# Optimization experiments

Hardware: AMD Instinct MI355X
Metric: run time of the kernel (lower is better)

The kernel has to match this reference:

```python
import jax, jax.numpy as jnp
import numpy as np

STRIDE = 1
PADDING = 1

def setup_inputs() -> dict:
    key = jax.random.key(0)
    k1, k2 = jax.random.split(key)
    X = jax.random.normal(k1, (32, 1024, 1024), dtype=jnp.float32)
    weight = jnp.array([[-1.0, -1.0, -1.0], [-1.0, 8.0, -1.0], [-1.0, -1.0, -1.0]], dtype=jnp.float32)
    return {"X": X, "weight": weight}

def reference(X, weight):
    # single-channel 2D cross-correlation, stride=1, padding=1
    # X: [B, M, N] -> lhs [B, 1, M, N]; weight: [u, v] -> rhs [1, 1, u, v]
    lhs = X[:, None, :, :]
    rhs = weight[None, None, :, :]
    out = jax.lax.conv_general_dilated(
        lhs, rhs,
        window_strides=(STRIDE, STRIDE),
        padding=[(PADDING, PADDING), (PADDING, PADDING)],
        dimension_numbers=("NCHW", "OIHW", "NCHW"),
    )
    return out[:, 0, :, :]  # [B, out_h, out_w]
```

## Files before the change

### kernel.cpp

```cpp
#include <hip/hip_runtime.h>

#define IMG_W 1024
#define IMG_H 1024
#define BATCH 32
#define ROWS 8

typedef float vfloat4 __attribute__((ext_vector_type(4)));

__global__ __launch_bounds__(256) void conv3x3_kernel(
    const float* __restrict__ X,
    const float* __restrict__ wt,
    float* __restrict__ out)
{
    const int y0 = blockIdx.x * ROWS;
    const int b  = blockIdx.y;
    const int c0 = threadIdx.x * 4;

    const float* img = X + (size_t)b * IMG_H * IMG_W;

    const float w0 = wt[0], w1 = wt[1], w2 = wt[2];
    const float w3 = wt[3], w4 = wt[4], w5 = wt[5];
    const float w6 = wt[6], w7 = wt[7], w8 = wt[8];

    float R[ROWS + 2][6];

#pragma unroll
    for (int i = 0; i < ROWS + 2; ++i) {
        const int ry = y0 + i - 1;
        if (ry >= 0 && ry < IMG_H) {
            const float* p = img + (size_t)ry * IMG_W + c0;
            const vfloat4 v = *(const vfloat4*)p;
            R[i][1] = v.x; R[i][2] = v.y; R[i][3] = v.z; R[i][4] = v.w;
            R[i][0] = (c0 > 0)         ? p[-1] : 0.f;
            R[i][5] = (c0 + 4 < IMG_W) ? p[4]  : 0.f;
        } else {
            R[i][0] = R[i][1] = R[i][2] = R[i][3] = R[i][4] = R[i][5] = 0.f;
        }
    }

    float* obase = out + ((size_t)b * IMG_H + y0) * IMG_W + c0;

#pragma unroll
    for (int i = 0; i < ROWS; ++i) {
        vfloat4 r;
#pragma unroll
        for (int j = 0; j < 4; ++j) {
            r[j] = w0 * R[i][j]     + w1 * R[i][j + 1]     + w2 * R[i][j + 2]
                 + w3 * R[i + 1][j] + w4 * R[i + 1][j + 1] + w5 * R[i + 1][j + 2]
                 + w6 * R[i + 2][j] + w7 * R[i + 2][j + 1] + w8 * R[i + 2][j + 2];
        }
        __builtin_nontemporal_store(r, (vfloat4*)(obase + (size_t)i * IMG_W));
    }
}

extern "C" void kernel_launch(void* const* d_in, const int* in_sizes, int n_in,
                              void* d_out, int out_size, void* d_ws, size_t ws_size,
                              hipStream_t stream) {
    const float* X  = (const float*)d_in[0];
    const float* wt = (const float*)d_in[1];
    float* out = (float*)d_out;

    dim3 grid(IMG_H / ROWS, BATCH);
    dim3 block(256);
    conv3x3_kernel<<<grid, block, 0, stream>>>(X, wt, out);
}
```

Before: 229.4 us.

## Use rolling 3-row register window with wave shuffles for column halos

Doubles rows per block to reduce vertical halo re-reads, replaces per-thread scalar halo loads with cross-lane shuffles (loading from memory only at wave edges), and keeps a rotating 3-row register buffer instead of all rows. It also raises the occupancy hint in launch bounds. This aims to cut redundant loads and register pressure, at the cost of fewer blocks in the grid and extra shuffle instructions.

```diff
diff --git a/kernel.cpp b/kernel.cpp
--- a/kernel.cpp
+++ b/kernel.cpp
@@ -3,18 +3,37 @@
 #define IMG_W 1024
 #define IMG_H 1024
 #define BATCH 32
-#define ROWS 8
+#define ROWS 16
 
 typedef float vfloat4 __attribute__((ext_vector_type(4)));
 
-__global__ __launch_bounds__(256) void conv3x3_kernel(
+__device__ __forceinline__ void load_row(const float* __restrict__ img,
+                                         int ry, int c0, int lane,
+                                         float (&R)[6])
+{
+    if (ry < 0 || ry >= IMG_H) {
+#pragma unroll
+        for (int k = 0; k < 6; ++k) R[k] = 0.f;
+        return;
+    }
+    const float* p = img + (size_t)ry * IMG_W + c0;
+    const vfloat4 v = *(const vfloat4*)p;
+    float left  = __shfl_up(v.w, 1);
+    float right = __shfl_down(v.x, 1);
+    if (lane == 0)  left  = (c0 > 0)         ? p[-1] : 0.f;
+    if (lane == 63) right = (c0 + 4 < IMG_W) ? p[4]  : 0.f;
+    R[0] = left; R[1] = v.x; R[2] = v.y; R[3] = v.z; R[4] = v.w; R[5] = right;
+}
+
+__global__ __launch_bounds__(256, 8) void conv3x3_kernel(
     const float* __restrict__ X,
     const float* __restrict__ wt,
     float* __restrict__ out)
 {
-    const int y0 = blockIdx.x * ROWS;
-    const int b  = blockIdx.y;
-    const int c0 = threadIdx.x * 4;
+    const int y0   = blockIdx.x * ROWS;
+    const int b    = blockIdx.y;
+    const int c0   = threadIdx.x * 4;
+    const int lane = threadIdx.x & 63;
 
     const float* img = X + (size_t)b * IMG_H * IMG_W;
 
@@ -22,32 +41,24 @@
     const float w3 = wt[3], w4 = wt[4], w5 = wt[5];
     const float w6 = wt[6], w7 = wt[7], w8 = wt[8];
 
-    float R[ROWS + 2][6];
-
-#pragma unroll
-    for (int i = 0; i < ROWS + 2; ++i) {
-        const int ry = y0 + i - 1;
-        if (ry >= 0 && ry < IMG_H) {
-            const float* p = img + (size_t)ry * IMG_W + c0;
-            const vfloat4 v = *(const vfloat4*)p;
-            R[i][1] = v.x; R[i][2] = v.y; R[i][3] = v.z; R[i][4] = v.w;
-            R[i][0] = (c0 > 0)         ? p[-1] : 0.f;
-            R[i][5] = (c0 + 4 < IMG_W) ? p[4]  : 0.f;
-        } else {
-            R[i][0] = R[i][1] = R[i][2] = R[i][3] = R[i][4] = R[i][5] = 0.f;
-        }
-    }
+    float R[3][6];
+    load_row(img, y0 - 1, c0, lane, R[0]);
+    load_row(img, y0,     c0, lane, R[1]);
 
     float* obase = out + ((size_t)b * IMG_H + y0) * IMG_W + c0;
 
 #pragma unroll
     for (int i = 0; i < ROWS; ++i) {
+        load_row(img, y0 + 1 + i, c0, lane, R[(i + 2) % 3]);
+        const float (&ra)[6] = R[i % 3];
+        const float (&rb)[6] = R[(i + 1) % 3];
+        const float (&rc)[6] = R[(i + 2) % 3];
         vfloat4 r;
 #pragma unroll
         for (int j = 0; j < 4; ++j) {
-            r[j] = w0 * R[i][j]     + w1 * R[i][j + 1]     + w2 * R[i][j + 2]
-                 + w3 * R[i + 1][j] + w4 * R[i + 1][j + 1] + w5 * R[i + 1][j + 2]
-                 + w6 * R[i + 2][j] + w7 * R[i + 2][j + 1] + w8 * R[i + 2][j + 2];
+            r[j] = w0 * ra[j] + w1 * ra[j + 1] + w2 * ra[j + 2]
+                 + w3 * rb[j] + w4 * rb[j + 1] + w5 * rb[j + 2]
+                 + w6 * rc[j] + w7 * rc[j + 1] + w8 * rc[j + 2];
         }
         __builtin_nontemporal_store(r, (vfloat4*)(obase + (size_t)i * IMG_W));
     }
```

After: 239.2 us. 1.04x slower.

## Use taller row tiles with rolling register buffer and shuffle-based halos

Applied to the files above, without the earlier changes.

Each block now processes 32 output rows with a 4-slot rolling buffer of input rows, issuing the next row's load while computing the current one. Left/right halo columns come from wave shuffles, with global loads only on wave-edge lanes. This cuts redundant row re-reads between tiles and the per-thread scalar halo loads. The trade-off is fewer blocks in flight, which may reduce latency hiding.

```diff
diff --git a/kernel.cpp b/kernel.cpp
--- a/kernel.cpp
+++ b/kernel.cpp
@@ -3,7 +3,8 @@
 #define IMG_W 1024
 #define IMG_H 1024
 #define BATCH 32
-#define ROWS 8
+#define TALL  32
+#define TILES_PER_IMG (IMG_H / TALL)
 
 typedef float vfloat4 __attribute__((ext_vector_type(4)));
 
@@ -12,9 +13,11 @@
     const float* __restrict__ wt,
     float* __restrict__ out)
 {
-    const int y0 = blockIdx.x * ROWS;
-    const int b  = blockIdx.y;
-    const int c0 = threadIdx.x * 4;
+    const int t    = blockIdx.x;
+    const int b    = t / TILES_PER_IMG;
+    const int y0   = (t % TILES_PER_IMG) * TALL;
+    const int c0   = threadIdx.x * 4;
+    const int lane = threadIdx.x & 63;
 
     const float* img = X + (size_t)b * IMG_H * IMG_W;
 
@@ -22,34 +25,58 @@
     const float w3 = wt[3], w4 = wt[4], w5 = wt[5];
     const float w6 = wt[6], w7 = wt[7], w8 = wt[8];
 
-    float R[ROWS + 2][6];
+    vfloat4 V[4];
+    float   HL[4], HR[4];
+    float   E[4][6];
+
+    auto issue = [&](int s, int ry) {
+        float hl = 0.f, hr = 0.f;
+        if (ry >= 0 && ry < IMG_H) {
+            const float* p = img + (size_t)ry * IMG_W + c0;
+            V[s] = *(const vfloat4*)p;
+            if (lane == 0  && c0 > 0)         hl = p[-1];
+            if (lane == 63 && c0 + 4 < IMG_W) hr = p[4];
+        } else {
+            V[s] = (vfloat4){0.f, 0.f, 0.f, 0.f};
+        }
+        HL[s] = hl; HR[s] = hr;
+    };
+
+    auto expand = [&](int s) {
+        float left  = __shfl_up(V[s].w, 1);
+        float right = __shfl_down(V[s].x, 1);
+        left  = (lane == 0)  ? HL[s] : left;
+        right = (lane == 63) ? HR[s] : right;
+        E[s][0] = left;    E[s][1] = V[s].x; E[s][2] = V[s].y;
+        E[s][3] = V[s].z;  E[s][4] = V[s].w; E[s][5] = right;
+    };
 
 #pragma unroll
-    for (int i = 0; i < ROWS + 2; ++i) {
-        const int ry = y0 + i - 1;
-        if (ry >= 0 && ry < IMG_H) {
-            const float* p = img + (size_t)ry * IMG_W + c0;
-            const vfloat4 v = *(const vfloat4*)p;
-            R[i][1] = v.x; R[i][2] = v.y; R[i][3] = v.z; R[i][4] = v.w;
-            R[i][0] = (c0 > 0)         ? p[-1] : 0.f;
-            R[i][5] = (c0 + 4 < IMG_W) ? p[4]  : 0.f;
-        } else {
-            R[i][0] = R[i][1] = R[i][2] = R[i][3] = R[i][4] = R[i][5] = 0.f;
-        }
-    }
+    for (int j = 0; j < 4; ++j) issue(j, y0 - 1 + j);
+    expand(0);
+    expand(1);
 
     float* obase = out + ((size_t)b * IMG_H + y0) * IMG_W + c0;
 
 #pragma unroll
-    for (int i = 0; i < ROWS; ++i) {
+    for (int i = 0; i < TALL; ++i) {
+        expand((i + 2) & 3);
+        const float (&ra)[6] = E[i & 3];
+        const float (&rb)[6] = E[(i + 1) & 3];
+        const float (&rc)[6] = E[(i + 2) & 3];
         vfloat4 r;
 #pragma unroll
         for (int j = 0; j < 4; ++j) {
-            r[j] = w0 * R[i][j]     + w1 * R[i][j + 1]     + w2 * R[i][j + 2]
-                 + w3 * R[i + 1][j] + w4 * R[i + 1][j + 1] + w5 * R[i + 1][j + 2]
-                 + w6 * R[i + 2][j] + w7 * R[i + 2][j + 1] + w8 * R[i + 2][j + 2];
+            r[j] = w0 * ra[j] + w1 * ra[j + 1] + w2 * ra[j + 2]
+                 + w3 * rb[j] + w4 * rb[j + 1] + w5 * rb[j + 2]
+                 + w6 * rc[j] + w7 * rc[j + 1] + w8 * rc[j + 2];
         }
         __builtin_nontemporal_store(r, (vfloat4*)(obase + (size_t)i * IMG_W));
+
+        if (i < TALL - 2) {
+            issue(i & 3, y0 + 3 + i);
+            asm volatile("" : "+v"(V[i & 3]), "+v"(HL[i & 3]), "+v"(HR[i & 3]));
+        }
     }
 }
 
@@ -60,7 +87,7 @@
     const float* wt = (const float*)d_in[1];
     float* out = (float*)d_out;
 
-    dim3 grid(IMG_H / ROWS, BATCH);
+    dim3 grid(TILES_PER_IMG * BATCH);
     dim3 block(256);
     conv3x3_kernel<<<grid, block, 0, stream>>>(X, wt, out);
 }
```

Result: slower. 239.5 us (+4.4%).
